# Optimization experiments

Measured on AMD Instinct MI355X. Metric: run time of the kernel, lower is better.

The kernel has to match this reference:

```python
import jax, jax.numpy as jnp
import numpy as np

KS = 3          # kernel size
PAD = 1         # padding
N = KS * KS     # number of sampling taps (9)


def setup_inputs() -> dict:
    key = jax.random.key(0)
    k0, k1, k2 = jax.random.split(key, 3)
    B, Cin, Cout, H, W = 4, 64, 64, 128, 128
    x = jax.random.normal(k0, (B, Cin, H, W), jnp.float32)
    # offset conv is zero-initialized in the original; use small random weights
    # so the sampling pattern is actually irregular (post-training behavior)
    w_off = jax.random.normal(k1, (2 * N, Cin, KS, KS), jnp.float32) * 0.05
    b_off = jnp.zeros((2 * N,), jnp.float32)
    w_def = jax.random.normal(k2, (Cout, Cin, KS, KS), jnp.float32) / np.float32(np.sqrt(Cin * N))
    b_def = jnp.zeros((Cout,), jnp.float32)
    return {"x": x, "w_off": w_off, "b_off": b_off, "w_def": w_def, "b_def": b_def}


def _conv3x3(x, w, b):
    y = jax.lax.conv_general_dilated(
        x, w, window_strides=(1, 1), padding=((PAD, PAD), (PAD, PAD)),
        dimension_numbers=("NCHW", "OIHW", "NCHW"))
    return y + b[None, :, None, None]


def _deform_forward(x, w_off, b_off, w_def, b_def):
    B, C, H, W = x.shape
    Cout = w_def.shape[0]
    offset = _conv3x3(x, w_off, b_off)                 # [B, 2N, H, W]

    xp = jnp.pad(x, ((0, 0), (0, 0), (PAD, PAD), (PAD, PAD)))  # zero pad
    Hp, Wp = H + 2 * PAD, W + 2 * PAD

    # sampling positions p = p0 + pn + offset (coords in padded frame)
    r = jnp.arange(-(KS // 2), KS // 2 + 1, dtype=x.dtype)
    pn_x = jnp.repeat(r, KS)          # [-1,-1,-1, 0,0,0, 1,1,1]
    pn_y = jnp.tile(r, KS)            # [-1, 0, 1, ...]
    p0x = jnp.arange(1, H + 1, dtype=x.dtype)[None, :, None, None]  # [1,H,1,1]
    p0y = jnp.arange(1, W + 1, dtype=x.dtype)[None, None, :, None]  # [1,1,W,1]
    offx = offset[:, :N].transpose(0, 2, 3, 1)          # [B,H,W,N]
    offy = offset[:, N:].transpose(0, 2, 3, 1)
    px = p0x + pn_x[None, None, None, :] + offx          # [B,H,W,N]
    py = p0y + pn_y[None, None, None, :] + offy

    # integer corners (floor has zero grad == detach in torch ref)
    flx, fly = jnp.floor(px), jnp.floor(py)
    qlx = jnp.clip(flx, 0, Hp - 1)
    qly = jnp.clip(fly, 0, Wp - 1)
    qrx = jnp.clip(flx + 1, 0, Hp - 1)
    qry = jnp.clip(fly + 1, 0, Wp - 1)
    pxc = jnp.clip(px, 0, Hp - 1)
    pyc = jnp.clip(py, 0, Wp - 1)

    # bilinear weights (matches torch DeformConv2D formulas)
    g_lt = (1 + (qlx - pxc)) * (1 + (qly - pyc))
    g_rb = (1 - (qrx - pxc)) * (1 - (qry - pyc))
    g_lb = (1 + (qlx - pxc)) * (1 - (qry - pyc))
    g_rt = (1 - (qrx - pxc)) * (1 + (qly - pyc))

    xf = xp.reshape(B, C, Hp * Wp)

    def gather(xfb, ix, iy):
        idx = (ix * Wp + iy).astype(jnp.int32).reshape(-1)
        return xfb[:, idx].reshape(C, H, W, N)

    g4 = jax.vmap(gather)
    x_lt = g4(xf, qlx, qly)   # [B,C,H,W,N]
    x_rb = g4(xf, qrx, qry)
    x_lb = g4(xf, qlx, qry)
    x_rt = g4(xf, qrx, qly)

    x_off = (g_lt[:, None] * x_lt + g_rb[:, None] * x_rb
             + g_lb[:, None] * x_lb + g_rt[:, None] * x_rt)  # [B,C,H,W,N]

    out = jnp.einsum("bchwn,ocn->bohw", x_off, w_def.reshape(Cout, C, N))
    return out + b_def[None, :, None, None]


def reference(x, w_off, b_off, w_def, b_def):
    return _deform_forward(x, w_off, b_off, w_def, b_def)
```

## Files before the change

kernel.cpp:

```cpp
#include <hip/hip_runtime.h>

#define B_   4
#define CIN  64
#define COUT 64
#define H_   128
#define W_   128
#define NOFF 18
#define HW   (H_ * W_)
#define HP   130
#define WP   130

typedef __attribute__((ext_vector_type(8))) short bf16x8;
typedef __attribute__((ext_vector_type(4))) float f32x4;

__device__ __forceinline__ unsigned short f2bf(float f) {
    unsigned int u = __float_as_uint(f);
    return (unsigned short)((u + 0x7fffu + ((u >> 16) & 1u)) >> 16);
}

__global__ __launch_bounds__(256) void k_wt(
    const float* __restrict__ w_def, const float* __restrict__ w_off,
    unsigned short* __restrict__ wB, unsigned short* __restrict__ wBo)
{
    const int i = blockIdx.x * 256 + threadIdx.x;
    if (i < 18 * 4 * 64) {
        const int kblk = i >> 8;
        const int nblk = (i >> 6) & 3;
        const int lane = i & 63;
        const int o = nblk * 16 + (lane & 15);
        unsigned int pk[4];
#pragma unroll
        for (int d = 0; d < 4; ++d) {
            unsigned int v = 0;
#pragma unroll
            for (int e = 0; e < 2; ++e) {
                const int K = kblk * 32 + 8 * (lane >> 4) + d * 2 + e;
                const int n = K >> 6, c = K & 63;
                v |= (unsigned int)f2bf(w_def[((size_t)o * 64 + c) * 9 + n]) << (16 * e);
            }
            pk[d] = v;
        }
        *(uint4*)(wB + (size_t)i * 8) = make_uint4(pk[0], pk[1], pk[2], pk[3]);
    }
    const int j = i - 18 * 4 * 64;
    if (j >= 0 && j < 18 * 2 * 64) {
        const int kblk = j >> 7;
        const int nblk = (j >> 6) & 1;
        const int lane = j & 63;
        const int o = nblk * 16 + (lane & 15);
        unsigned int pk[4];
#pragma unroll
        for (int d = 0; d < 4; ++d) {
            unsigned int v = 0;
#pragma unroll
            for (int e = 0; e < 2; ++e) {
                const int K = kblk * 32 + 8 * (lane >> 4) + d * 2 + e;
                const int n = K >> 6, c = K & 63;
                const float wv = (o < NOFF) ? w_off[((size_t)o * 64 + c) * 9 + n] : 0.f;
                v |= (unsigned int)f2bf(wv) << (16 * e);
            }
            pk[d] = v;
        }
        *(uint4*)(wBo + (size_t)j * 8) = make_uint4(pk[0], pk[1], pk[2], pk[3]);
    }
}

__global__ __launch_bounds__(256) void k_xt(
    const float* __restrict__ x, unsigned short* __restrict__ xt)
{
    const int b  = blockIdx.x / HP;
    const int hp = blockIdx.x - b * HP;
    const int c  = threadIdx.x & 63;
    const int wq = threadIdx.x >> 6;
    unsigned short* dst = xt + (((size_t)b * HP + hp) * WP) * 64 + c;
    for (int wp = wq; wp < WP; wp += 4) {
        float v = 0.f;
        if (hp >= 1 && hp <= H_ && wp >= 1 && wp <= W_)
            v = x[(((size_t)b * CIN + c) * H_ + (hp - 1)) * W_ + (wp - 1)];
        dst[(size_t)wp * 64] = f2bf(v);
    }
}

__global__ __launch_bounds__(256) void k_xt2(
    const unsigned short* __restrict__ xt, unsigned int* __restrict__ xt2)
{
    const int b  = blockIdx.x / HP;
    const int hp = blockIdx.x - b * HP;
    const int c  = threadIdx.x & 63;
    const int wq = threadIdx.x >> 6;
    const unsigned short* src = xt + (((size_t)b * HP + hp) * WP) * 64 + c;
    unsigned int* dst = xt2 + (((size_t)b * HP + hp) * WP) * 64 + c;
    for (int wp = wq; wp < WP; wp += 4) {
        unsigned int lo = src[(size_t)wp * 64];
        unsigned int hi = (wp + 1 < WP) ? (unsigned int)src[(size_t)(wp + 1) * 64] : 0u;
        dst[(size_t)wp * 64] = lo | (hi << 16);
    }
}

__global__ __launch_bounds__(256) void k_offconv_mfma(
    const unsigned short* __restrict__ xt, const unsigned short* __restrict__ wBo,
    const float* __restrict__ b_off, float* __restrict__ off)
{
    const int tid  = threadIdx.x;
    const int lane = tid & 63;
    const int wv   = tid >> 6;
    const int row  = lane & 15;
    const int g    = lane >> 4;

    const int lb = ((blockIdx.x & 7) << 7) | (blockIdx.x >> 3);

    const int p0 = lb * 64 + wv * 16;
    const int b  = p0 >> 14;
    const int h  = (p0 >> 7) & 127;
    const int w0 = p0 & 127;

    const unsigned short* xtb = xt + (size_t)b * (HP * WP * 64);
    const unsigned short* Bp  = wBo + (size_t)lane * 8;

    f32x4 acc0 = {0.f, 0.f, 0.f, 0.f};
    f32x4 acc1 = {0.f, 0.f, 0.f, 0.f};

#pragma unroll
    for (int kb = 0; kb < 18; ++kb) {
        const int n  = kb >> 1;
        const int hp = h + n / 3;
        const int wp = w0 + row + (n % 3);
        const int cb = (kb & 1) * 32 + g * 8;
        const bf16x8 a  = *(const bf16x8*)(xtb + ((size_t)hp * WP + wp) * 64 + cb);
        const bf16x8 b0 = *(const bf16x8*)(Bp + (size_t)(kb * 2 + 0) * 512);
        const bf16x8 b1 = *(const bf16x8*)(Bp + (size_t)(kb * 2 + 1) * 512);
        acc0 = __builtin_amdgcn_mfma_f32_16x16x32_bf16(a, b0, acc0, 0, 0, 0);
        acc1 = __builtin_amdgcn_mfma_f32_16x16x32_bf16(a, b1, acc1, 0, 0, 0);
    }

    const int hwb = (p0 + 4 * g) & 16383;
    {
        const int o = row;
        float4 v = make_float4(acc0[0] + b_off[o], acc0[1] + b_off[o],
                               acc0[2] + b_off[o], acc0[3] + b_off[o]);
        *(float4*)&off[((size_t)b * NOFF + o) * HW + hwb] = v;
    }
    if (row < 2) {
        const int o = 16 + row;
        float4 v = make_float4(acc1[0] + b_off[o], acc1[1] + b_off[o],
                               acc1[2] + b_off[o], acc1[3] + b_off[o]);
        *(float4*)&off[((size_t)b * NOFF + o) * HW + hwb] = v;
    }
}

__global__ __launch_bounds__(256) void k_fuse(
    const unsigned int* __restrict__ xt2, const float* __restrict__ off,
    unsigned short* __restrict__ xoff, const unsigned short* __restrict__ wB,
    const float* __restrict__ b_def, float* __restrict__ out)
{
    const int tid   = threadIdx.x;
    const int lane  = tid & 63;
    const int wv    = tid >> 6;
    const int pxblk = ((blockIdx.x & 7) << 8) | (blockIdx.x >> 3);
    const int b     = pxblk >> 9;
    const int h     = (pxblk >> 2) & 127;
    const int w0    = (pxblk & 3) * 32;

    __shared__ uint2  geoI[9][32];
    __shared__ float4 geoG[9][32];

    if (lane < 32) {
        const int wpix = w0 + lane;
        const float* offp = off + ((size_t)b * NOFF) * HW + h * W_ + wpix;
        for (int n = wv; n < 9; n += 4) {
            const float ox = offp[(size_t)n * HW];
            const float oy = offp[(size_t)(n + 9) * HW];
            const float px = (float)(h + n / 3) + ox;
            const float py = (float)(wpix + n % 3) + oy;
            const float flx = floorf(px), fly = floorf(py);
            const float qlx = fminf(fmaxf(flx, 0.f), 129.f);
            const float qly = fminf(fmaxf(fly, 0.f), 129.f);
            const float qrx = fminf(fmaxf(flx + 1.f, 0.f), 129.f);
            const float qry = fminf(fmaxf(fly + 1.f, 0.f), 129.f);
            const float pxc = fminf(fmaxf(px, 0.f), 129.f);
            const float pyc = fminf(fmaxf(py, 0.f), 129.f);
            const float gxl = 1.f + (qlx - pxc);
            const float gxr = 1.f - (qrx - pxc);
            const float gyl = 1.f + (qly - pyc);
            const float gyr = 1.f - (qry - pyc);
            const int xl = (int)qlx, yl = (int)qly, xr = (int)qrx, yr = (int)qry;
            float wyl = gyl, wyr = gyr;
            if (yr == yl) { wyl = gyl + gyr; wyr = 0.f; }
            geoI[n][lane] = make_uint2((unsigned)((xl * WP + yl) * 256),
                                       (unsigned)((xr * WP + yl) * 256));
            geoG[n][lane] = make_float4(wyl, wyr, gxl, gxr);
        }
    }
    __syncthreads();

    const char* xtb4 = (const char*)(xt2 + (size_t)b * (HP * WP * 64)) + lane * 4;
    unsigned short* xo = xoff + (size_t)(pxblk * 32) * 576;

#pragma unroll 1
    for (int pxi = 0; pxi < 8; ++pxi) {
        const int pxl = wv * 8 + pxi;
#pragma unroll 3
        for (int n = 0; n < 9; ++n) {
            const uint2  gi = geoI[n][pxl];
            const float4 gg = geoG[n][pxl];
            const unsigned int u1 = *(const unsigned int*)(xtb4 + gi.x);
            const unsigned int u2 = *(const unsigned int*)(xtb4 + gi.y);
            const float s0 = __uint_as_float(u1 << 16);
            const float s1 = __uint_as_float(u1 & 0xffff0000u);
            const float t0 = __uint_as_float(u2 << 16);
            const float t1 = __uint_as_float(u2 & 0xffff0000u);
            const float r1 = fmaf(gg.x, s0, gg.y * s1);
            const float r2 = fmaf(gg.x, t0, gg.y * t1);
            const float v  = fmaf(gg.z, r1, gg.w * r2);
            xo[(size_t)pxl * 576 + n * 64 + lane] = f2bf(v);
        }
    }

    __syncthreads();
    if (wv >= 2) return;

    const int row = lane & 15;
    const int g   = lane >> 4;

    const unsigned short* Ap = xoff + (size_t)(pxblk * 32 + wv * 16 + row) * 576 + g * 8;
    const unsigned short* Bp = wB + (size_t)lane * 8;

    f32x4 acc0 = {0.f, 0.f, 0.f, 0.f};
    f32x4 acc1 = {0.f, 0.f, 0.f, 0.f};
    f32x4 acc2 = {0.f, 0.f, 0.f, 0.f};
    f32x4 acc3 = {0.f, 0.f, 0.f, 0.f};

#pragma unroll 3
    for (int kb = 0; kb < 18; ++kb) {
        const bf16x8 a  = *(const bf16x8*)(Ap + kb * 32);
        const bf16x8 b0 = *(const bf16x8*)(Bp + (size_t)(kb * 4 + 0) * 512);
        const bf16x8 b1 = *(const bf16x8*)(Bp + (size_t)(kb * 4 + 1) * 512);
        const bf16x8 b2 = *(const bf16x8*)(Bp + (size_t)(kb * 4 + 2) * 512);
        const bf16x8 b3 = *(const bf16x8*)(Bp + (size_t)(kb * 4 + 3) * 512);
        acc0 = __builtin_amdgcn_mfma_f32_16x16x32_bf16(a, b0, acc0, 0, 0, 0);
        acc1 = __builtin_amdgcn_mfma_f32_16x16x32_bf16(a, b1, acc1, 0, 0, 0);
        acc2 = __builtin_amdgcn_mfma_f32_16x16x32_bf16(a, b2, acc2, 0, 0, 0);
        acc3 = __builtin_amdgcn_mfma_f32_16x16x32_bf16(a, b3, acc3, 0, 0, 0);
    }

    const int p_base = pxblk * 32 + wv * 16 + 4 * g;
#pragma unroll
    for (int i = 0; i < 4; ++i) {
        const int o = i * 16 + row;
        const float bias = b_def[o];
        const f32x4 A = (i == 0) ? acc0 : (i == 1) ? acc1 : (i == 2) ? acc2 : acc3;
#pragma unroll
        for (int r = 0; r < 4; ++r) {
            const int p  = p_base + r;
            const int bb = p >> 14;
            const int hw = p & 16383;
            out[((size_t)(bb * COUT + o)) * HW + hw] = A[r] + bias;
        }
    }
}

extern "C" void kernel_launch(void* const* d_in, const int* in_sizes, int n_in,
                              void* d_out, int out_size, void* d_ws, size_t ws_size,
                              hipStream_t stream)
{
    const float* x     = (const float*)d_in[0];
    const float* w_off = (const float*)d_in[1];
    const float* b_off = (const float*)d_in[2];
    const float* w_def = (const float*)d_in[3];
    const float* b_def = (const float*)d_in[4];
    float* out = (float*)d_out;

    char* ws = (char*)d_ws;
    float*          off  = (float*)(ws + 0);
    unsigned short* wB   = (unsigned short*)(ws + 4718592);
    unsigned short* wBo  = (unsigned short*)(ws + 4792320);
    unsigned short* xt   = (unsigned short*)(ws + 4829184);
    unsigned int*   xt2  = (unsigned int*)(ws + 13481984);
    unsigned short* xoff = (unsigned short*)(ws + 30787584);

    k_wt<<<(18 * 4 * 64 + 18 * 2 * 64 + 255) / 256, 256, 0, stream>>>(
        w_def, w_off, wB, wBo);
    k_xt<<<B_ * HP, 256, 0, stream>>>(x, xt);
    k_xt2<<<B_ * HP, 256, 0, stream>>>(xt, xt2);
    k_offconv_mfma<<<B_ * HW / 64, 256, 0, stream>>>(xt, wBo, b_off, off);
    k_fuse<<<B_ * HW / 32, 256, 0, stream>>>(xt2, off, xoff, wB, b_def, out);
}
```

Baseline: 94.26 us.

## Fuse layout prep kernels and merge offset conv into deform kernel

```diff
diff --git a/kernel.cpp b/kernel.cpp
--- a/kernel.cpp
+++ b/kernel.cpp
@@ -65,140 +65,115 @@
     }
 }
 
-__global__ __launch_bounds__(256) void k_xt(
-    const float* __restrict__ x, unsigned short* __restrict__ xt)
+__global__ __launch_bounds__(256) void k_prep(
+    const float* __restrict__ x, unsigned short* __restrict__ xt,
+    unsigned int* __restrict__ xt2)
 {
     const int b  = blockIdx.x / HP;
     const int hp = blockIdx.x - b * HP;
     const int c  = threadIdx.x & 63;
     const int wq = threadIdx.x >> 6;
-    unsigned short* dst = xt + (((size_t)b * HP + hp) * WP) * 64 + c;
+    const float* xr = x + (((size_t)b * CIN + c) * H_ + (hp - 1)) * W_;
+    unsigned short* d1 = xt  + (((size_t)b * HP + hp) * WP) * 64 + c;
+    unsigned int*   d2 = xt2 + (((size_t)b * HP + hp) * WP) * 64 + c;
+    const bool hin = (hp >= 1 && hp <= H_);
     for (int wp = wq; wp < WP; wp += 4) {
-        float v = 0.f;
-        if (hp >= 1 && hp <= H_ && wp >= 1 && wp <= W_)
-            v = x[(((size_t)b * CIN + c) * H_ + (hp - 1)) * W_ + (wp - 1)];
-        dst[(size_t)wp * 64] = f2bf(v);
-    }
-}
-
-__global__ __launch_bounds__(256) void k_xt2(
-    const unsigned short* __restrict__ xt, unsigned int* __restrict__ xt2)
-{
-    const int b  = blockIdx.x / HP;
-    const int hp = blockIdx.x - b * HP;
-    const int c  = threadIdx.x & 63;
-    const int wq = threadIdx.x >> 6;
-    const unsigned short* src = xt + (((size_t)b * HP + hp) * WP) * 64 + c;
-    unsigned int* dst = xt2 + (((size_t)b * HP + hp) * WP) * 64 + c;
-    for (int wp = wq; wp < WP; wp += 4) {
-        unsigned int lo = src[(size_t)wp * 64];
-        unsigned int hi = (wp + 1 < WP) ? (unsigned int)src[(size_t)(wp + 1) * 64] : 0u;
-        dst[(size_t)wp * 64] = lo | (hi << 16);
-    }
-}
-
-__global__ __launch_bounds__(256) void k_offconv_mfma(
-    const unsigned short* __restrict__ xt, const unsigned short* __restrict__ wBo,
-    const float* __restrict__ b_off, float* __restrict__ off)
-{
-    const int tid  = threadIdx.x;
-    const int lane = tid & 63;
-    const int wv   = tid >> 6;
-    const int row  = lane & 15;
-    const int g    = lane >> 4;
-
-    const int lb = ((blockIdx.x & 7) << 7) | (blockIdx.x >> 3);
-
-    const int p0 = lb * 64 + wv * 16;
-    const int b  = p0 >> 14;
-    const int h  = (p0 >> 7) & 127;
-    const int w0 = p0 & 127;
-
-    const unsigned short* xtb = xt + (size_t)b * (HP * WP * 64);
-    const unsigned short* Bp  = wBo + (size_t)lane * 8;
-
-    f32x4 acc0 = {0.f, 0.f, 0.f, 0.f};
-    f32x4 acc1 = {0.f, 0.f, 0.f, 0.f};
-
-#pragma unroll
-    for (int kb = 0; kb < 18; ++kb) {
-        const int n  = kb >> 1;
-        const int hp = h + n / 3;
-        const int wp = w0 + row + (n % 3);
-        const int cb = (kb & 1) * 32 + g * 8;
-        const bf16x8 a  = *(const bf16x8*)(xtb + ((size_t)hp * WP + wp) * 64 + cb);
-        const bf16x8 b0 = *(const bf16x8*)(Bp + (size_t)(kb * 2 + 0) * 512);
-        const bf16x8 b1 = *(const bf16x8*)(Bp + (size_t)(kb * 2 + 1) * 512);
-        acc0 = __builtin_amdgcn_mfma_f32_16x16x32_bf16(a, b0, acc0, 0, 0, 0);
-        acc1 = __builtin_amdgcn_mfma_f32_16x16x32_bf16(a, b1, acc1, 0, 0, 0);
-    }
-
-    const int hwb = (p0 + 4 * g) & 16383;
-    {
-        const int o = row;
-        float4 v = make_float4(acc0[0] + b_off[o], acc0[1] + b_off[o],
-                               acc0[2] + b_off[o], acc0[3] + b_off[o]);
-        *(float4*)&off[((size_t)b * NOFF + o) * HW + hwb] = v;
-    }
-    if (row < 2) {
-        const int o = 16 + row;
-        float4 v = make_float4(acc1[0] + b_off[o], acc1[1] + b_off[o],
-                               acc1[2] + b_off[o], acc1[3] + b_off[o]);
-        *(float4*)&off[((size_t)b * NOFF + o) * HW + hwb] = v;
-    }
-}
-
-__global__ __launch_bounds__(256) void k_fuse(
-    const unsigned int* __restrict__ xt2, const float* __restrict__ off,
-    unsigned short* __restrict__ xoff, const unsigned short* __restrict__ wB,
-    const float* __restrict__ b_def, float* __restrict__ out)
-{
+        float v1 = 0.f, v2 = 0.f;
+        if (hin) {
+            if (wp >= 1 && wp <= W_)       v1 = xr[wp - 1];
+            if (wp + 1 >= 1 && wp + 1 <= W_) v2 = xr[wp];
+        }
+        const unsigned int a1 = f2bf(v1), a2 = f2bf(v2);
+        d1[(size_t)wp * 64] = (unsigned short)a1;
+        d2[(size_t)wp * 64] = a1 | (a2 << 16);
+    }
+}
+
+__global__ __launch_bounds__(256) void k_mega(
+    const unsigned short* __restrict__ xt, const unsigned int* __restrict__ xt2,
+    const unsigned short* __restrict__ wBo, const unsigned short* __restrict__ wB,
+    const float* __restrict__ b_off, const float* __restrict__ b_def,
+    unsigned short* __restrict__ xoff, float* __restrict__ out)
+{
+    __shared__ float  off_s[NOFF][64];
+    __shared__ uint2  geoI[9][64];
+    __shared__ float4 geoG[9][64];
+
     const int tid   = threadIdx.x;
     const int lane  = tid & 63;
     const int wv    = tid >> 6;
-    const int pxblk = ((blockIdx.x & 7) << 8) | (blockIdx.x >> 3);
-    const int b     = pxblk >> 9;
-    const int h     = (pxblk >> 2) & 127;
-    const int w0    = (pxblk & 3) * 32;
-
-    __shared__ uint2  geoI[9][32];
-    __shared__ float4 geoG[9][32];
-
-    if (lane < 32) {
-        const int wpix = w0 + lane;
-        const float* offp = off + ((size_t)b * NOFF) * HW + h * W_ + wpix;
-        for (int n = wv; n < 9; n += 4) {
-            const float ox = offp[(size_t)n * HW];
-            const float oy = offp[(size_t)(n + 9) * HW];
-            const float px = (float)(h + n / 3) + ox;
-            const float py = (float)(wpix + n % 3) + oy;
-            const float flx = floorf(px), fly = floorf(py);
-            const float qlx = fminf(fmaxf(flx, 0.f), 129.f);
-            const float qly = fminf(fmaxf(fly, 0.f), 129.f);
-            const float qrx = fminf(fmaxf(flx + 1.f, 0.f), 129.f);
-            const float qry = fminf(fmaxf(fly + 1.f, 0.f), 129.f);
-            const float pxc = fminf(fmaxf(px, 0.f), 129.f);
-            const float pyc = fminf(fmaxf(py, 0.f), 129.f);
-            const float gxl = 1.f + (qlx - pxc);
-            const float gxr = 1.f - (qrx - pxc);
-            const float gyl = 1.f + (qly - pyc);
-            const float gyr = 1.f - (qry - pyc);
-            const int xl = (int)qlx, yl = (int)qly, xr = (int)qrx, yr = (int)qry;
-            float wyl = gyl, wyr = gyr;
-            if (yr == yl) { wyl = gyl + gyr; wyr = 0.f; }
-            geoI[n][lane] = make_uint2((unsigned)((xl * WP + yl) * 256),
-                                       (unsigned)((xr * WP + yl) * 256));
-            geoG[n][lane] = make_float4(wyl, wyr, gxl, gxr);
+    const int row   = lane & 15;
+    const int g     = lane >> 4;
+    const int pxblk = blockIdx.x;
+    const int b     = pxblk >> 8;
+    const int h     = (pxblk >> 1) & 127;
+    const int w0    = (pxblk & 1) * 64;
+
+    {
+        const unsigned short* xtb = xt + (size_t)b * (HP * WP * 64);
+        const unsigned short* Bp  = wBo + (size_t)lane * 8;
+        f32x4 acc0 = {0.f, 0.f, 0.f, 0.f};
+        f32x4 acc1 = {0.f, 0.f, 0.f, 0.f};
+#pragma unroll
+        for (int kb = 0; kb < 18; ++kb) {
+            const int n  = kb >> 1;
+            const int hp = h + n / 3;
+            const int wp = w0 + wv * 16 + row + (n % 3);
+            const int cb = (kb & 1) * 32 + g * 8;
+            const bf16x8 a  = *(const bf16x8*)(xtb + ((size_t)hp * WP + wp) * 64 + cb);
+            const bf16x8 b0 = *(const bf16x8*)(Bp + (size_t)(kb * 2 + 0) * 512);
+            const bf16x8 b1 = *(const bf16x8*)(Bp + (size_t)(kb * 2 + 1) * 512);
+            acc0 = __builtin_amdgcn_mfma_f32_16x16x32_bf16(a, b0, acc0, 0, 0, 0);
+            acc1 = __builtin_amdgcn_mfma_f32_16x16x32_bf16(a, b1, acc1, 0, 0, 0);
+        }
+        const int pxb = wv * 16 + 4 * g;
+        {
+            const float bias = b_off[row];
+#pragma unroll
+            for (int r = 0; r < 4; ++r) off_s[row][pxb + r] = acc0[r] + bias;
+        }
+        if (row < 2) {
+            const float bias = b_off[16 + row];
+#pragma unroll
+            for (int r = 0; r < 4; ++r) off_s[16 + row][pxb + r] = acc1[r] + bias;
         }
     }
     __syncthreads();
 
+    for (int it = tid; it < 576; it += 256) {
+        const int pxl = it & 63;
+        const int n   = it >> 6;
+        const int wpix = w0 + pxl;
+        const float ox = off_s[n][pxl];
+        const float oy = off_s[n + 9][pxl];
+        const float px = (float)(h + n / 3) + ox;
+        const float py = (float)(wpix + n % 3) + oy;
+        const float flx = floorf(px), fly = floorf(py);
+        const float qlx = fminf(fmaxf(flx, 0.f), 129.f);
+        const float qly = fminf(fmaxf(fly, 0.f), 129.f);
+        const float qrx = fminf(fmaxf(flx + 1.f, 0.f), 129.f);
+        const float qry = fminf(fmaxf(fly + 1.f, 0.f), 129.f);
+        const float pxc = fminf(fmaxf(px, 0.f), 129.f);
+        const float pyc = fminf(fmaxf(py, 0.f), 129.f);
+        const float gxl = 1.f + (qlx - pxc);
+        const float gxr = 1.f - (qrx - pxc);
+        const float gyl = 1.f + (qly - pyc);
+        const float gyr = 1.f - (qry - pyc);
+        const int xl = (int)qlx, yl = (int)qly, xr = (int)qrx, yr = (int)qry;
+        float wyl = gyl, wyr = gyr;
+        if (yr == yl) { wyl = gyl + gyr; wyr = 0.f; }
+        geoI[n][pxl] = make_uint2((unsigned)((xl * WP + yl) * 256),
+                                  (unsigned)((xr * WP + yl) * 256));
+        geoG[n][pxl] = make_float4(wyl, wyr, gxl, gxr);
+    }
+    __syncthreads();
+
     const char* xtb4 = (const char*)(xt2 + (size_t)b * (HP * WP * 64)) + lane * 4;
-    unsigned short* xo = xoff + (size_t)(pxblk * 32) * 576;
+    unsigned short* xo = xoff + (size_t)(pxblk * 64) * 576;
 
 #pragma unroll 1
-    for (int pxi = 0; pxi < 8; ++pxi) {
-        const int pxl = wv * 8 + pxi;
+    for (int pxi = 0; pxi < 16; ++pxi) {
+        const int pxl = wv * 16 + pxi;
 #pragma unroll 3
         for (int n = 0; n < 9; ++n) {
             const uint2  gi = geoI[n][pxl];
@@ -217,12 +192,8 @@
     }
 
     __syncthreads();
-    if (wv >= 2) return;
-
-    const int row = lane & 15;
-    const int g   = lane >> 4;
-
-    const unsigned short* Ap = xoff + (size_t)(pxblk * 32 + wv * 16 + row) * 576 + g * 8;
+
+    const unsigned short* Ap = xoff + (size_t)(pxblk * 64 + wv * 16 + row) * 576 + g * 8;
     const unsigned short* Bp = wB + (size_t)lane * 8;
 
     f32x4 acc0 = {0.f, 0.f, 0.f, 0.f};
@@ -243,7 +214,7 @@
         acc3 = __builtin_amdgcn_mfma_f32_16x16x32_bf16(a, b3, acc3, 0, 0, 0);
     }
 
-    const int p_base = pxblk * 32 + wv * 16 + 4 * g;
+    const int p_base = pxblk * 64 + wv * 16 + 4 * g;
 #pragma unroll
     for (int i = 0; i < 4; ++i) {
         const int o = i * 16 + row;
@@ -271,17 +242,15 @@
     float* out = (float*)d_out;
 
     char* ws = (char*)d_ws;
-    float*          off  = (float*)(ws + 0);
-    unsigned short* wB   = (unsigned short*)(ws + 4718592);
-    unsigned short* wBo  = (unsigned short*)(ws + 4792320);
-    unsigned short* xt   = (unsigned short*)(ws + 4829184);
-    unsigned int*   xt2  = (unsigned int*)(ws + 13481984);
-    unsigned short* xoff = (unsigned short*)(ws + 30787584);
+    unsigned short* wB   = (unsigned short*)(ws + 0);
+    unsigned short* wBo  = (unsigned short*)(ws + 73728);
+    unsigned short* xt   = (unsigned short*)(ws + 110592);
+    unsigned int*   xt2  = (unsigned int*)(ws + 8763392);
+    unsigned short* xoff = (unsigned short*)(ws + 26068992);
 
     k_wt<<<(18 * 4 * 64 + 18 * 2 * 64 + 255) / 256, 256, 0, stream>>>(
         w_def, w_off, wB, wBo);
-    k_xt<<<B_ * HP, 256, 0, stream>>>(x, xt);
-    k_xt2<<<B_ * HP, 256, 0, stream>>>(xt, xt2);
-    k_offconv_mfma<<<B_ * HW / 64, 256, 0, stream>>>(xt, wBo, b_off, off);
-    k_fuse<<<B_ * HW / 32, 256, 0, stream>>>(xt2, off, xoff, wB, b_def, out);
-}
+    k_prep<<<B_ * HP, 256, 0, stream>>>(x, xt, xt2);
+    k_mega<<<B_ * HW / 64, 256, 0, stream>>>(xt, xt2, wBo, wB, b_off, b_def,
+                                             xoff, out);
+}
```

After: 95.03 us. Within noise of the previous version (+0.8%).
